# Kernel optimization log

Hardware: AMD Instinct MI355X
Metric: run time of the kernel (lower is better)

The kernel has to match this reference:

```python
import jax, jax.numpy as jnp
import numpy as np

N = 100_000      # nodes
E = 3_200_000    # edges
H = 32           # hidden_dim
L = 4            # num_layers
G = 1_000        # graphs in batch
F_IN = 1         # num_features
C = 2            # num_classes
BN_EPS = 1e-5


def setup_inputs() -> dict:
    key = jax.random.key(0)
    ks = jax.random.split(key, 8)
    s = 0.1  # param init scale
    x = jax.random.normal(ks[0], (N, F_IN), jnp.float32)
    edge_index = jax.random.randint(ks[1], (2, E), 0, N, dtype=jnp.int64)
    batch = jnp.sort(jax.random.randint(ks[2], (N,), 0, G, dtype=jnp.int64))
    return {
        "x": x,
        "edge_index": edge_index,
        "batch": batch,
        "W_enc": jax.random.normal(ks[3], (F_IN, H), jnp.float32) * s,
        "b_enc": jnp.zeros((H,), jnp.float32),
        "eps": jnp.zeros((L,), jnp.float32),           # GIN train_eps, init 0
        "W1": jax.random.normal(ks[4], (L, H, H), jnp.float32) * s,
        "b1": jnp.zeros((L, H), jnp.float32),
        "W2": jax.random.normal(ks[5], (L, H, H), jnp.float32) * s,
        "b2": jnp.zeros((L, H), jnp.float32),
        "gamma": jnp.ones((L, H), jnp.float32),
        "beta": jnp.zeros((L, H), jnp.float32),
        "W_cls": jax.random.normal(ks[6], (H, C), jnp.float32) * s,
        "b_cls": jnp.zeros((C,), jnp.float32),
    }


def reference(x, edge_index, batch, W_enc, b_enc, eps, W1, b1, W2, b2,
              gamma, beta, W_cls, b_cls):
    h = x @ W_enc + b_enc                      # [N, H] node encoder
    src, dst = edge_index[0], edge_index[1]    # message flow src -> dst
    for l in range(L):
        # GINConv: (1+eps)*x + sum_{j in N(i)} x_j
        agg = jax.ops.segment_sum(h[src], dst, num_segments=N)   # [N, H]
        z = (1.0 + eps[l]) * h + agg
        # 2-layer MLP
        z = jnp.maximum(z @ W1[l] + b1[l], 0.0) @ W2[l] + b2[l]
        # BatchNorm1d (training-mode batch statistics over nodes)
        mu = z.mean(axis=0)
        var = z.var(axis=0)
        z = gamma[l] * (z - mu) * jax.lax.rsqrt(var + BN_EPS) + beta[l]
        h = jnp.maximum(z, 0.0)                # ReLU (dropout = identity, eval)
    pooled = jax.ops.segment_sum(h, batch, num_segments=G)   # global_add_pool
    return pooled @ W_cls + b_cls              # [G, C]
```

## Files before the change

### kernel.cpp

```cpp
#include <hip/hip_runtime.h>

#define N_NODES 100000
#define N_EDGES 3200000
#define HD      32
#define NLAYERS 4
#define NGRAPHS 1000
#define BN_EPS  1e-5f
#define BSHIFT  9
#define NBUCK   ((N_NODES + 511) >> 9)
#define PCHUNK  8192
#define NPB     ((N_EDGES + PCHUNK - 1) / PCHUNK)
#define ENC_BLOCKS ((N_NODES * 8 + 255) / 256)

typedef _Float16 f16;
typedef _Float16 f16x8 __attribute__((ext_vector_type(8)));
typedef float    f32x4 __attribute__((ext_vector_type(4)));
typedef int      i32x4 __attribute__((ext_vector_type(4)));
typedef unsigned char uc4 __attribute__((ext_vector_type(4)));
typedef unsigned char uc8 __attribute__((ext_vector_type(8)));

__global__ __launch_bounds__(256) void k_encphist(
    const float* __restrict__ x, const float* __restrict__ W_enc,
    const float* __restrict__ b_enc, const int* __restrict__ ei,
    unsigned char* __restrict__ hq, float* __restrict__ stats,
    float* __restrict__ pooled, int* __restrict__ pcnt)
{
    __shared__ int hist[256];
    int bb = blockIdx.x, t = threadIdx.x;
    if (bb < NPB) {
        hist[t] = 0;
        __syncthreads();
        int base4 = bb * (PCHUNK / 4);
        int n4 = min(PCHUNK / 4, N_EDGES / 4 - base4);
        const i32x4* d4 = (const i32x4*)(ei + N_EDGES);
        for (int k = t; k < n4; k += 256) {
            i32x4 d = __builtin_nontemporal_load(d4 + base4 + k);
            atomicAdd(&hist[d.x >> BSHIFT], 1);
            atomicAdd(&hist[d.y >> BSHIFT], 1);
            atomicAdd(&hist[d.z >> BSHIFT], 1);
            atomicAdd(&hist[d.w >> BSHIFT], 1);
        }
        __syncthreads();
        pcnt[t * NPB + bb] = hist[t];
    } else {
        int gid = (bb - NPB) * 256 + t;
        if (gid < NLAYERS * 64)   stats[gid]  = 0.f;
        if (gid < NGRAPHS * HD)   pooled[gid] = 0.f;
        if (gid < N_NODES * 8) {
            int i = gid >> 3, c0 = (gid & 7) * 4;
            float xv = x[i];
            uc4 r;
            #pragma unroll
            for (int k = 0; k < 4; ++k) {
                float w = W_enc[c0 + k];
                float s = 5.5f * fabsf(w) / 127.f + 1e-8f;
                int q = (int)rintf(xv * w / s) + 128;
                q = max(0, min(255, q));
                r[k] = (unsigned char)q;
            }
            *(uc4*)(hq + i * 32 + c0) = r;
        }
    }
}

__global__ __launch_bounds__(512) void k_pscanA(int* __restrict__ pcnt,
                                                int* __restrict__ btot)
{
    __shared__ int sc[2][512];
    int t = threadIdx.x, b = blockIdx.x;
    int base = b * NPB;
    int v = (t < NPB) ? pcnt[base + t] : 0;
    int pp = 0;
    sc[0][t] = v;
    __syncthreads();
    for (int st = 1; st < 512; st <<= 1) {
        int x = sc[pp][t];
        if (t >= st) x += sc[pp][t - st];
        sc[pp ^ 1][t] = x;
        pp ^= 1;
        __syncthreads();
    }
    int incl = sc[pp][t];
    if (t < NPB) pcnt[base + t] = incl - v;
    if (t == NPB - 1) btot[b] = incl;
}

__global__ __launch_bounds__(256) void k_pscatter(const int* __restrict__ ei,
                                                  const int* __restrict__ pcnt,
                                                  const int* __restrict__ btot,
                                                  unsigned int* __restrict__ ebuf)
{
    __shared__ int sb[2][256];
    __shared__ int lcur[256];
    int t = threadIdx.x, blk = blockIdx.x;
    sb[0][t] = (t < NBUCK) ? btot[t] : 0;
    __syncthreads();
    int pp = 0;
    for (int st = 1; st < 256; st <<= 1) {
        int v = sb[pp][t];
        if (t >= st) v += sb[pp][t - st];
        sb[pp ^ 1][t] = v;
        pp ^= 1;
        __syncthreads();
    }
    int bexcl = (t == 0) ? 0 : sb[pp][t - 1];
    lcur[t] = pcnt[t * NPB + blk] + bexcl;
    __syncthreads();
    int base4 = blk * (PCHUNK / 4);
    int n4 = min(PCHUNK / 4, N_EDGES / 4 - base4);
    const i32x4* s4 = (const i32x4*)ei;
    const i32x4* d4 = (const i32x4*)(ei + N_EDGES);
    for (int k = t; k < n4; k += 256) {
        i32x4 s = __builtin_nontemporal_load(s4 + base4 + k);
        i32x4 d = __builtin_nontemporal_load(d4 + base4 + k);
        int pos;
        pos = atomicAdd(&lcur[d.x >> BSHIFT], 1);
        ebuf[pos] = ((unsigned)s.x << BSHIFT) | (unsigned)(d.x & 511);
        pos = atomicAdd(&lcur[d.y >> BSHIFT], 1);
        ebuf[pos] = ((unsigned)s.y << BSHIFT) | (unsigned)(d.y & 511);
        pos = atomicAdd(&lcur[d.z >> BSHIFT], 1);
        ebuf[pos] = ((unsigned)s.z << BSHIFT) | (unsigned)(d.z & 511);
        pos = atomicAdd(&lcur[d.w >> BSHIFT], 1);
        ebuf[pos] = ((unsigned)s.w << BSHIFT) | (unsigned)(d.w & 511);
    }
}

__global__ __launch_bounds__(512) void k_bfinal(const unsigned int* __restrict__ ebuf,
                                                const int* __restrict__ btot,
                                                int* __restrict__ off,
                                                int* __restrict__ csr)
{
    __shared__ int sb[2][256];
    __shared__ int cnt[512], scanbuf[2][512], cur[512];
    int tid = threadIdx.x, b = blockIdx.x;
    if (tid < 256) sb[0][tid] = (tid < NBUCK) ? btot[tid] : 0;
    __syncthreads();
    int pp = 0;
    for (int st = 1; st < 256; st <<= 1) {
        if (tid < 256) {
            int v = sb[pp][tid];
            if (tid >= st) v += sb[pp][tid - st];
            sb[pp ^ 1][tid] = v;
        }
        pp ^= 1;
        __syncthreads();
    }
    int base = (b == 0) ? 0 : sb[pp][b - 1];
    int nE = sb[pp][b] - base;
    if (b == NBUCK - 1 && tid == 0) off[N_NODES] = sb[pp][NBUCK - 1];
    cnt[tid] = 0;
    __syncthreads();
    for (int e = tid; e < nE; e += 512)
        atomicAdd(&cnt[ebuf[base + e] & 511], 1);
    __syncthreads();
    int p2 = 0;
    scanbuf[0][tid] = cnt[tid];
    __syncthreads();
    for (int st = 1; st < 512; st <<= 1) {
        int v = scanbuf[p2][tid];
        if (tid >= st) v += scanbuf[p2][tid - st];
        scanbuf[p2 ^ 1][tid] = v;
        p2 ^= 1;
        __syncthreads();
    }
    int excl = scanbuf[p2][tid] - cnt[tid];
    cur[tid] = excl;
    int gnode = (b << BSHIFT) + tid;
    if (gnode < N_NODES) off[gnode] = base + excl;
    __syncthreads();
    for (int e = tid; e < nE; e += 512) {
        unsigned int p = ebuf[base + e];
        int pos = atomicAdd(&cur[p & 511], 1);
        csr[base + pos] = (int)(p >> BSHIFT);
    }
}

__global__ __launch_bounds__(256) void k_layer(
    const unsigned char* __restrict__ hq, const int* __restrict__ off,
    const int* __restrict__ csr, const float* __restrict__ epsArr,
    const float* __restrict__ gamma, const float* __restrict__ beta,
    const float* __restrict__ W_enc, const float* __restrict__ b_enc,
    const float* __restrict__ W1, const float* __restrict__ b1,
    const float* __restrict__ W2, const float* __restrict__ b2,
    f16* __restrict__ z2out, float* __restrict__ stats, int layer)
{
    __shared__ float T[4][16 * 36];
    __shared__ float redS[4][32], redQ[4][32];
    int tid = threadIdx.x, wave = tid >> 6, lane = tid & 63;
    int col = lane & 15, quad = lane >> 4;
    float dq_s[8], dq_o[8];
    if (layer == 0) {
        #pragma unroll
        for (int k = 0; k < 8; ++k) {
            int ch = quad * 8 + k;
            float w = W_enc[ch];
            float s = 5.5f * fabsf(w) / 127.f + 1e-8f;
            dq_s[k] = s;
            dq_o[k] = b_enc[ch] - 128.f * s;
        }
    } else {
        #pragma unroll
        for (int k = 0; k < 8; ++k) {
            int ch = quad * 8 + k;
            float g = gamma[(layer - 1) * 32 + ch];
            float bb = beta[(layer - 1) * 32 + ch];
            float vmax = fmaxf(bb + 5.5f * fabsf(g), 0.f);
            dq_s[k] = fmaxf(vmax, 1e-6f) / 255.f;
            dq_o[k] = 0.f;
        }
    }
    float oneEps = 1.f + epsArr[layer];
    const float* W1l = W1 + layer * 1024;
    const float* W2l = W2 + layer * 1024;
    f16x8 w1a, w1b, w2a, w2b;
    #pragma unroll
    for (int j = 0; j < 8; ++j) {
        int k = quad * 8 + j;
        w1a[j] = (f16)W1l[k * 32 + col];
        w1b[j] = (f16)W1l[k * 32 + col + 16];
        w2a[j] = (f16)W2l[k * 32 + col];
        w2b[j] = (f16)W2l[k * 32 + col + 16];
    }
    float b1a = b1[layer * 32 + col], b1b = b1[layer * 32 + col + 16];
    float b2a = b2[layer * 32 + col], b2b = b2[layer * 32 + col + 16];
    f32x4 bias1a = {b1a, b1a, b1a, b1a}, bias1b = {b1b, b1b, b1b, b1b};
    f32x4 bias2a = {b2a, b2a, b2a, b2a}, bias2b = {b2b, b2b, b2b, b2b};
    float* Tw = T[wave];

    float sA = 0.f, qA = 0.f, sB = 0.f, qB = 0.f;
    const int NT = N_NODES / 16;

    for (int tile = blockIdx.x * 4 + wave; tile < NT; tile += gridDim.x * 4) {
        int nb = tile * 16;
        int node = nb + col;
        int j = off[node], jend = off[node + 1];
        float deg = (float)(jend - j);
        f32x4 A0 = {0,0,0,0}, A1 = {0,0,0,0}, B0 = {0,0,0,0}, B1 = {0,0,0,0};
        while (j + 4 <= jend) {
            int s0 = csr[j], s1 = csr[j+1], s2 = csr[j+2], s3 = csr[j+3];
            uc8 g0 = *(const uc8*)(hq + s0 * 32 + quad * 8);
            uc8 g1 = *(const uc8*)(hq + s1 * 32 + quad * 8);
            uc8 g2 = *(const uc8*)(hq + s2 * 32 + quad * 8);
            uc8 g3 = *(const uc8*)(hq + s3 * 32 + quad * 8);
            #pragma unroll
            for (int k = 0; k < 4; ++k) {
                A0[k] += (float)g0[k]     + (float)g2[k];
                A1[k] += (float)g0[k + 4] + (float)g2[k + 4];
                B0[k] += (float)g1[k]     + (float)g3[k];
                B1[k] += (float)g1[k + 4] + (float)g3[k + 4];
            }
            j += 4;
        }
        while (j < jend) {
            uc8 g = *(const uc8*)(hq + csr[j] * 32 + quad * 8);
            #pragma unroll
            for (int k = 0; k < 4; ++k) {
                A0[k] += (float)g[k];
                A1[k] += (float)g[k + 4];
            }
            ++j;
        }
        uc8 gs = *(const uc8*)(hq + node * 32 + quad * 8);
        float degE = deg + oneEps;
        f16x8 a;
        #pragma unroll
        for (int k = 0; k < 4; ++k) {
            float F0 = A0[k] + B0[k] + oneEps * (float)gs[k];
            float F1 = A1[k] + B1[k] + oneEps * (float)gs[k + 4];
            a[k]     = (f16)(dq_s[k]     * F0 + dq_o[k]     * degE);
            a[k + 4] = (f16)(dq_s[k + 4] * F1 + dq_o[k + 4] * degE);
        }
        f32x4 m0 = __builtin_amdgcn_mfma_f32_16x16x32_f16(a, w1a, bias1a, 0, 0, 0);
        f32x4 m1 = __builtin_amdgcn_mfma_f32_16x16x32_f16(a, w1b, bias1b, 0, 0, 0);
        #pragma unroll
        for (int r = 0; r < 4; ++r) {
            int row = quad * 4 + r;
            Tw[row * 36 + col]      = fmaxf(m0[r], 0.f);
            Tw[row * 36 + col + 16] = fmaxf(m1[r], 0.f);
        }
        f32x4 t0 = *(const f32x4*)(Tw + col * 36 + quad * 8);
        f32x4 t1 = *(const f32x4*)(Tw + col * 36 + quad * 8 + 4);
        f16x8 a2;
        #pragma unroll
        for (int k = 0; k < 4; ++k) { a2[k] = (f16)t0[k]; a2[k + 4] = (f16)t1[k]; }
        f32x4 z0 = __builtin_amdgcn_mfma_f32_16x16x32_f16(a2, w2a, bias2a, 0, 0, 0);
        f32x4 zb = __builtin_amdgcn_mfma_f32_16x16x32_f16(a2, w2b, bias2b, 0, 0, 0);
        #pragma unroll
        for (int r = 0; r < 4; ++r) {
            int n2 = nb + quad * 4 + r;
            z2out[n2 * 32 + col]      = (f16)z0[r];
            z2out[n2 * 32 + col + 16] = (f16)zb[r];
            sA += z0[r]; qA += z0[r] * z0[r];
            sB += zb[r]; qB += zb[r] * zb[r];
        }
    }

    sA += __shfl_xor(sA, 16); sA += __shfl_xor(sA, 32);
    qA += __shfl_xor(qA, 16); qA += __shfl_xor(qA, 32);
    sB += __shfl_xor(sB, 16); sB += __shfl_xor(sB, 32);
    qB += __shfl_xor(qB, 16); qB += __shfl_xor(qB, 32);
    if (lane < 16) {
        redS[wave][col] = sA; redS[wave][col + 16] = sB;
        redQ[wave][col] = qA; redQ[wave][col + 16] = qB;
    }
    __syncthreads();
    if (tid < 64) {
        int sel = tid >> 5, cc = tid & 31;
        float s = 0.f;
        #pragma unroll
        for (int w = 0; w < 4; ++w) s += sel ? redQ[w][cc] : redS[w][cc];
        atomicAdd(&stats[layer * 64 + sel * 32 + cc], s);
    }
}

__global__ __launch_bounds__(256) void k_quant(
    const f16* __restrict__ z2, const float* __restrict__ stats,
    const float* __restrict__ gamma, const float* __restrict__ beta,
    unsigned char* __restrict__ hq, int layer)
{
    int idx = blockIdx.x * 256 + threadIdx.x;
    if (idx >= N_NODES * 4) return;
    int c0 = (idx & 3) * 8;
    const float invN = 1.0f / (float)N_NODES;
    float bnsc[8], bnsh[8], inv_s[8];
    #pragma unroll
    for (int k = 0; k < 8; ++k) {
        int ch = c0 + k;
        float g = gamma[layer * 32 + ch], bb = beta[layer * 32 + ch];
        float mu  = stats[layer * 64 + ch] * invN;
        float var = stats[layer * 64 + 32 + ch] * invN - mu * mu;
        float sc = g * rsqrtf(var + BN_EPS);
        bnsc[k] = sc;
        bnsh[k] = bb - mu * sc;
        float vmax = fmaxf(bb + 5.5f * fabsf(g), 0.f);
        inv_s[k] = 255.f / fmaxf(vmax, 1e-6f);
    }
    f16x8 z = *(const f16x8*)(z2 + (size_t)idx * 8);
    uc8 r;
    #pragma unroll
    for (int k = 0; k < 8; ++k) {
        float v = fmaxf(fmaf((float)z[k], bnsc[k], bnsh[k]), 0.f);
        int q = (int)(fminf(v * inv_s[k], 255.f) + 0.5f);
        r[k] = (unsigned char)q;
    }
    __builtin_nontemporal_store(r, (uc8*)(hq + (size_t)idx * 8));
}

__global__ __launch_bounds__(256) void k_pool(const f16* __restrict__ z2,
                                              const int* __restrict__ batch,
                                              const float* __restrict__ stats,
                                              const float* __restrict__ gamma,
                                              const float* __restrict__ beta,
                                              float* __restrict__ pooled)
{
    int c = threadIdx.x & 31, slot = threadIdx.x >> 5;
    const float invN = 1.0f / (float)N_NODES;
    float mu  = stats[3 * 64 + c] * invN;
    float var = stats[3 * 64 + 32 + c] * invN - mu * mu;
    float sc = gamma[3 * 32 + c] * rsqrtf(var + BN_EPS);
    float sh = beta[3 * 32 + c] - mu * sc;
    int start = blockIdx.x * 256 + slot * 32;
    if (start >= N_NODES) return;
    int end = min(start + 32, N_NODES);
    int cur = batch[start]; float acc = 0.f;
    for (int i = start; i < end; ++i) {
        int g = batch[i];
        if (g != cur) { atomicAdd(&pooled[cur * HD + c], acc); acc = 0.f; cur = g; }
        acc += fmaxf(fmaf((float)z2[i * 32 + c], sc, sh), 0.f);
    }
    atomicAdd(&pooled[cur * HD + c], acc);
}

__global__ __launch_bounds__(256) void k_cls(const float* __restrict__ pooled,
                                             const float* __restrict__ Wc,
                                             const float* __restrict__ bc,
                                             float* __restrict__ out)
{
    int gid = blockIdx.x * 256 + threadIdx.x;
    if (gid >= NGRAPHS * 2) return;
    int g = gid >> 1, c = gid & 1;
    float s = bc[c];
    #pragma unroll
    for (int k = 0; k < 32; ++k) s = fmaf(pooled[g * 32 + k], Wc[k * 2 + c], s);
    out[gid] = s;
}

extern "C" void kernel_launch(void* const* d_in, const int* in_sizes, int n_in,
                              void* d_out, int out_size, void* d_ws, size_t ws_size,
                              hipStream_t stream)
{
    const float* x      = (const float*)d_in[0];
    const int*   ei     = (const int*)d_in[1];
    const int*   batch  = (const int*)d_in[2];
    const float* W_enc  = (const float*)d_in[3];
    const float* b_enc  = (const float*)d_in[4];
    const float* epsArr = (const float*)d_in[5];
    const float* W1     = (const float*)d_in[6];
    const float* b1     = (const float*)d_in[7];
    const float* W2     = (const float*)d_in[8];
    const float* b2     = (const float*)d_in[9];
    const float* gamma  = (const float*)d_in[10];
    const float* beta   = (const float*)d_in[11];
    const float* Wc     = (const float*)d_in[12];
    const float* bc     = (const float*)d_in[13];
    float* out = (float*)d_out;

    char* ws = (char*)d_ws;
    size_t o = 0;
    auto alloc = [&](size_t bytes) {
        char* p = ws + o;
        o += (bytes + 255) & ~(size_t)255;
        return p;
    };
    unsigned char* hq = (unsigned char*)alloc((size_t)N_NODES * 32);
    f16*   z2     = (f16*) alloc((size_t)N_NODES * 32 * 2);
    int*   csr    = (int*) alloc((size_t)N_EDGES * 4);
    unsigned int* ebuf = (unsigned int*)alloc((size_t)N_EDGES * 4);
    int*   offA   = (int*) alloc((size_t)(N_NODES + 1) * 4);
    int*   pcnt   = (int*) alloc((size_t)256 * NPB * 4);
    int*   btot   = (int*) alloc(1024);
    float* stats  = (float*)alloc(NLAYERS * 64 * 4);
    float* pooled = (float*)alloc((size_t)NGRAPHS * HD * 4);

    k_encphist<<<NPB + ENC_BLOCKS, 256, 0, stream>>>(x, W_enc, b_enc, ei, hq,
                                                     stats, pooled, pcnt);
    k_pscanA  <<<NBUCK, 512, 0, stream>>>(pcnt, btot);
    k_pscatter<<<NPB, 256, 0, stream>>>(ei, pcnt, btot, ebuf);
    k_bfinal  <<<NBUCK, 512, 0, stream>>>(ebuf, btot, offA, csr);

    for (int l = 0; l < NLAYERS; ++l) {
        k_layer<<<1563, 256, 0, stream>>>(hq, offA, csr, epsArr, gamma, beta,
                                          W_enc, b_enc, W1, b1, W2, b2,
                                          z2, stats, l);
        if (l < NLAYERS - 1)
            k_quant<<<(N_NODES * 4 + 255) / 256, 256, 0, stream>>>(z2, stats,
                                                                   gamma, beta,
                                                                   hq, l);
    }
    k_pool<<<(N_NODES + 255) / 256, 256, 0, stream>>>(z2, batch, stats,
                                                      gamma, beta, pooled);
    k_cls <<<8, 256, 0, stream>>>(pooled, Wc, bc, out);
}
```

Baseline: 466.9 us.

## Split fused GIN layer into separate aggregation and MLP kernels with packed-int accumulation

The fused per-layer kernel is split into two kernels. An aggregation kernel maps 4 threads per node, loads CSR indices as aligned vectors, and accumulates uint8 features with packed 16-bit SIMD-within-register adds. It writes fp16 aggregated features to a new buffer. A separate MFMA MLP kernel then reads them. This decouples irregular gather work from the matrix work and drops the per-element float conversions, at the cost of an extra fp16 round trip through global memory and one more launch per layer. The packed 16-bit lanes could overflow only if a node's degree exceeds about 257.

```diff
diff --git a/kernel.cpp b/kernel.cpp
--- a/kernel.cpp
+++ b/kernel.cpp
@@ -16,6 +16,7 @@
 typedef _Float16 f16x8 __attribute__((ext_vector_type(8)));
 typedef float    f32x4 __attribute__((ext_vector_type(4)));
 typedef int      i32x4 __attribute__((ext_vector_type(4)));
+typedef unsigned int  u32x2 __attribute__((ext_vector_type(2)));
 typedef unsigned char uc4 __attribute__((ext_vector_type(4)));
 typedef unsigned char uc8 __attribute__((ext_vector_type(8)));
 
@@ -175,24 +176,23 @@
     }
 }
 
-__global__ __launch_bounds__(256) void k_layer(
+__global__ __launch_bounds__(256) void k_agg(
     const unsigned char* __restrict__ hq, const int* __restrict__ off,
     const int* __restrict__ csr, const float* __restrict__ epsArr,
     const float* __restrict__ gamma, const float* __restrict__ beta,
     const float* __restrict__ W_enc, const float* __restrict__ b_enc,
-    const float* __restrict__ W1, const float* __restrict__ b1,
-    const float* __restrict__ W2, const float* __restrict__ b2,
-    f16* __restrict__ z2out, float* __restrict__ stats, int layer)
-{
-    __shared__ float T[4][16 * 36];
-    __shared__ float redS[4][32], redQ[4][32];
-    int tid = threadIdx.x, wave = tid >> 6, lane = tid & 63;
-    int col = lane & 15, quad = lane >> 4;
+    f16* __restrict__ z1, int layer)
+{
+    int tid = threadIdx.x;
+    int unit = tid >> 2, li = tid & 3;
+    int node = blockIdx.x * 64 + unit;
+    if (node >= N_NODES) return;
+    int co = li * 8;
     float dq_s[8], dq_o[8];
     if (layer == 0) {
         #pragma unroll
         for (int k = 0; k < 8; ++k) {
-            int ch = quad * 8 + k;
+            int ch = co + k;
             float w = W_enc[ch];
             float s = 5.5f * fabsf(w) / 127.f + 1e-8f;
             dq_s[k] = s;
@@ -201,7 +201,7 @@
     } else {
         #pragma unroll
         for (int k = 0; k < 8; ++k) {
-            int ch = quad * 8 + k;
+            int ch = co + k;
             float g = gamma[(layer - 1) * 32 + ch];
             float bb = beta[(layer - 1) * 32 + ch];
             float vmax = fmaxf(bb + 5.5f * fabsf(g), 0.f);
@@ -210,6 +210,76 @@
         }
     }
     float oneEps = 1.f + epsArr[layer];
+    const unsigned MASK = 0x00FF00FFu;
+
+    int j = off[node], jend = off[node + 1];
+    float deg = (float)(jend - j);
+    unsigned a0 = 0, a1 = 0, a2 = 0, a3 = 0;
+    auto accum = [&](u32x2 v) {
+        a0 += v.x & MASK; a1 += (v.x >> 8) & MASK;
+        a2 += v.y & MASK; a3 += (v.y >> 8) & MASK;
+    };
+    while (j < jend && (j & 3))
+        accum(*(const u32x2*)(hq + csr[j++] * 32 + co));
+    int n8 = (jend - j) >> 3;
+    for (int it = 0; it < n8; ++it) {
+        i32x4 q0 = __builtin_nontemporal_load((const i32x4*)(csr + j));
+        i32x4 q1 = __builtin_nontemporal_load((const i32x4*)(csr + j + 4));
+        u32x2 g0 = *(const u32x2*)(hq + q0.x * 32 + co);
+        u32x2 g1 = *(const u32x2*)(hq + q0.y * 32 + co);
+        u32x2 g2 = *(const u32x2*)(hq + q0.z * 32 + co);
+        u32x2 g3 = *(const u32x2*)(hq + q0.w * 32 + co);
+        u32x2 g4 = *(const u32x2*)(hq + q1.x * 32 + co);
+        u32x2 g5 = *(const u32x2*)(hq + q1.y * 32 + co);
+        u32x2 g6 = *(const u32x2*)(hq + q1.z * 32 + co);
+        u32x2 g7 = *(const u32x2*)(hq + q1.w * 32 + co);
+        accum(g0); accum(g1); accum(g2); accum(g3);
+        accum(g4); accum(g5); accum(g6); accum(g7);
+        j += 8;
+    }
+    if (jend - j >= 4) {
+        i32x4 q0 = *(const i32x4*)(csr + j);
+        accum(*(const u32x2*)(hq + q0.x * 32 + co));
+        accum(*(const u32x2*)(hq + q0.y * 32 + co));
+        accum(*(const u32x2*)(hq + q0.z * 32 + co));
+        accum(*(const u32x2*)(hq + q0.w * 32 + co));
+        j += 4;
+    }
+    while (j < jend)
+        accum(*(const u32x2*)(hq + csr[j++] * 32 + co));
+
+    u32x2 gs = *(const u32x2*)(hq + node * 32 + co);
+    float F[8];
+    F[0] = (float)(a0 & 0xFFFF); F[2] = (float)(a0 >> 16);
+    F[1] = (float)(a1 & 0xFFFF); F[3] = (float)(a1 >> 16);
+    F[4] = (float)(a2 & 0xFFFF); F[6] = (float)(a2 >> 16);
+    F[5] = (float)(a3 & 0xFFFF); F[7] = (float)(a3 >> 16);
+    float qs[8];
+    #pragma unroll
+    for (int k = 0; k < 4; ++k) {
+        qs[k]     = (float)((gs.x >> (8 * k)) & 255u);
+        qs[k + 4] = (float)((gs.y >> (8 * k)) & 255u);
+    }
+    float degE = deg + oneEps;
+    f16x8 r;
+    #pragma unroll
+    for (int k = 0; k < 8; ++k) {
+        float Fk = F[k] + oneEps * qs[k];
+        r[k] = (f16)(fmaf(dq_s[k], Fk, dq_o[k] * degE));
+    }
+    *(f16x8*)(z1 + (size_t)node * 32 + co) = r;
+}
+
+__global__ __launch_bounds__(256) void k_mlp(
+    const f16* __restrict__ z1, const float* __restrict__ W1,
+    const float* __restrict__ b1, const float* __restrict__ W2,
+    const float* __restrict__ b2, f16* __restrict__ z2out,
+    float* __restrict__ stats, int layer)
+{
+    __shared__ float T[4][16 * 36];
+    __shared__ float redS[4][32], redQ[4][32];
+    int tid = threadIdx.x, wave = tid >> 6, lane = tid & 63;
+    int col = lane & 15, quad = lane >> 4;
     const float* W1l = W1 + layer * 1024;
     const float* W2l = W2 + layer * 1024;
     f16x8 w1a, w1b, w2a, w2b;
@@ -227,49 +297,13 @@
     f32x4 bias2a = {b2a, b2a, b2a, b2a}, bias2b = {b2b, b2b, b2b, b2b};
     float* Tw = T[wave];
 
+    const int NT = N_NODES / 16;
+    int gw = blockIdx.x * 4 + wave, nw = gridDim.x * 4;
     float sA = 0.f, qA = 0.f, sB = 0.f, qB = 0.f;
-    const int NT = N_NODES / 16;
-
-    for (int tile = blockIdx.x * 4 + wave; tile < NT; tile += gridDim.x * 4) {
+
+    for (int tile = gw; tile < NT; tile += nw) {
         int nb = tile * 16;
-        int node = nb + col;
-        int j = off[node], jend = off[node + 1];
-        float deg = (float)(jend - j);
-        f32x4 A0 = {0,0,0,0}, A1 = {0,0,0,0}, B0 = {0,0,0,0}, B1 = {0,0,0,0};
-        while (j + 4 <= jend) {
-            int s0 = csr[j], s1 = csr[j+1], s2 = csr[j+2], s3 = csr[j+3];
-            uc8 g0 = *(const uc8*)(hq + s0 * 32 + quad * 8);
-            uc8 g1 = *(const uc8*)(hq + s1 * 32 + quad * 8);
-            uc8 g2 = *(const uc8*)(hq + s2 * 32 + quad * 8);
-            uc8 g3 = *(const uc8*)(hq + s3 * 32 + quad * 8);
-            #pragma unroll
-            for (int k = 0; k < 4; ++k) {
-                A0[k] += (float)g0[k]     + (float)g2[k];
-                A1[k] += (float)g0[k + 4] + (float)g2[k + 4];
-                B0[k] += (float)g1[k]     + (float)g3[k];
-                B1[k] += (float)g1[k + 4] + (float)g3[k + 4];
-            }
-            j += 4;
-        }
-        while (j < jend) {
-            uc8 g = *(const uc8*)(hq + csr[j] * 32 + quad * 8);
-            #pragma unroll
-            for (int k = 0; k < 4; ++k) {
-                A0[k] += (float)g[k];
-                A1[k] += (float)g[k + 4];
-            }
-            ++j;
-        }
-        uc8 gs = *(const uc8*)(hq + node * 32 + quad * 8);
-        float degE = deg + oneEps;
-        f16x8 a;
-        #pragma unroll
-        for (int k = 0; k < 4; ++k) {
-            float F0 = A0[k] + B0[k] + oneEps * (float)gs[k];
-            float F1 = A1[k] + B1[k] + oneEps * (float)gs[k + 4];
-            a[k]     = (f16)(dq_s[k]     * F0 + dq_o[k]     * degE);
-            a[k + 4] = (f16)(dq_s[k + 4] * F1 + dq_o[k + 4] * degE);
-        }
+        f16x8 a = *(const f16x8*)(z1 + (size_t)(nb + col) * 32 + quad * 8);
         f32x4 m0 = __builtin_amdgcn_mfma_f32_16x16x32_f16(a, w1a, bias1a, 0, 0, 0);
         f32x4 m1 = __builtin_amdgcn_mfma_f32_16x16x32_f16(a, w1b, bias1b, 0, 0, 0);
         #pragma unroll
@@ -287,9 +321,9 @@
         f32x4 zb = __builtin_amdgcn_mfma_f32_16x16x32_f16(a2, w2b, bias2b, 0, 0, 0);
         #pragma unroll
         for (int r = 0; r < 4; ++r) {
-            int n2 = nb + quad * 4 + r;
-            z2out[n2 * 32 + col]      = (f16)z0[r];
-            z2out[n2 * 32 + col + 16] = (f16)zb[r];
+            int node = nb + quad * 4 + r;
+            z2out[node * 32 + col]      = (f16)z0[r];
+            z2out[node * 32 + col + 16] = (f16)zb[r];
             sA += z0[r]; qA += z0[r] * z0[r];
             sB += zb[r]; qB += zb[r] * zb[r];
         }
@@ -413,6 +447,7 @@
         return p;
     };
     unsigned char* hq = (unsigned char*)alloc((size_t)N_NODES * 32);
+    f16*   z1     = (f16*) alloc((size_t)N_NODES * 32 * 2);
     f16*   z2     = (f16*) alloc((size_t)N_NODES * 32 * 2);
     int*   csr    = (int*) alloc((size_t)N_EDGES * 4);
     unsigned int* ebuf = (unsigned int*)alloc((size_t)N_EDGES * 4);
@@ -429,9 +464,10 @@
     k_bfinal  <<<NBUCK, 512, 0, stream>>>(ebuf, btot, offA, csr);
 
     for (int l = 0; l < NLAYERS; ++l) {
-        k_layer<<<1563, 256, 0, stream>>>(hq, offA, csr, epsArr, gamma, beta,
-                                          W_enc, b_enc, W1, b1, W2, b2,
-                                          z2, stats, l);
+        k_agg<<<(N_NODES + 63) / 64, 256, 0, stream>>>(hq, offA, csr, epsArr,
+                                                       gamma, beta, W_enc, b_enc,
+                                                       z1, l);
+        k_mlp<<<782, 256, 0, stream>>>(z1, W1, b1, W2, b2, z2, stats, l);
         if (l < NLAYERS - 1)
             k_quant<<<(N_NODES * 4 + 255) / 256, 256, 0, stream>>>(z2, stats,
                                                                    gamma, beta,
```

Result: faster. 438.7 us, median of 2 (-6.0%).
